# Optimization experiments

Measured on AMD Instinct MI355X. Metric: run time of the kernel, lower is better.

Reference implementation:

```python
import jax, jax.numpy as jnp
import numpy as np


def setup_inputs() -> dict:
    key = jax.random.key(0)
    ks = jax.random.split(key, 9)
    B, C, H, W = 4, 256, 128, 128
    d = C // 8
    x = jax.random.normal(ks[0], (B, C, H, W), jnp.float32)
    wq = jax.random.normal(ks[1], (d, C), jnp.float32) * 0.05
    bq = jax.random.normal(ks[2], (d,), jnp.float32) * 0.05
    wk = jax.random.normal(ks[3], (d, C), jnp.float32) * 0.05
    bk = jax.random.normal(ks[4], (d,), jnp.float32) * 0.05
    wv = jax.random.normal(ks[5], (d, C), jnp.float32) * 0.05
    bv = jax.random.normal(ks[6], (d,), jnp.float32) * 0.05
    wp = jax.random.normal(ks[7], (C, d, 3, 3), jnp.float32) * 0.05
    gamma = jax.random.normal(ks[8], (1,), jnp.float32)
    return dict(x=x, wq=wq, bq=bq, wk=wk, bk=bk, wv=wv, bv=bv, wp=wp, gamma=gamma)


def reference(x, wq, bq, wk, bk, wv, bv, wp, gamma):
    B, C, H, W = x.shape
    d = wq.shape[0]  # C // 8
    N = H * W
    # 1x1 convs expressed as channel matmuls
    q = jnp.einsum('bchw,dc->bdhw', x, wq) + bq[None, :, None, None]
    k = jnp.einsum('bchw,dc->bdhw', x, wk) + bk[None, :, None, None]
    v = jnp.einsum('bchw,dc->bdhw', x, wv) + bv[None, :, None, None]
    Q = q.reshape(B, d, N)
    K = k.reshape(B, d, N)
    V = v.reshape(B, d, N)
    # channel-channel energy: [B, d, d]
    energy = jnp.einsum('bdn,ben->bde', Q, K)
    energy_new = jnp.max(energy, axis=-1, keepdims=True) - energy
    attention = jax.nn.softmax(energy_new, axis=-1)
    out = jnp.einsum('bde,ben->bdn', attention, V).reshape(B, d, H, W)
    # 3x3 conv (no bias) + exact GELU
    out = jax.lax.conv_general_dilated(
        out, wp, window_strides=(1, 1), padding='SAME',
        dimension_numbers=('NCHW', 'OIHW', 'NCHW'))
    out = jax.nn.gelu(out, approximate=False)
    return gamma[0] * out + x
```

## Files before the change

kernel.cpp:

```cpp
#include <hip/hip_runtime.h>
#include <hip/hip_bf16.h>
#include <math.h>

#define BB 4
#define CC 256
#define HH 128
#define WW 128
#define NN (HH*WW)
#define DD 32

#define AOT_CI   44
#define AOT_ROWE (130*AOT_CI)
#define AOT_IMGE (130*AOT_ROWE)
#define AOT_BYTES ((size_t)BB*AOT_IMGE*2)
#define AOT_ALLOC (AOT_BYTES + 1024)

#define WT_BYTES (9*256*AOT_CI*2)

#define PATCH_SZ 45760
#define WSLAB    22528
#define CONV_LDS (PATCH_SZ + 2*WSLAB)
#define EPI_PITCH 260

#define ASWZ_BYTES 98304
#define QKPITCH 36

typedef __attribute__((ext_vector_type(8)))  short bf16x8;
typedef __attribute__((ext_vector_type(4)))  float f32x4;
typedef __attribute__((ext_vector_type(16))) float f32x16;

__device__ inline void async_copy16(void* lds, const void* g) {
    __builtin_amdgcn_global_load_lds(
        (const __attribute__((address_space(1))) unsigned int*)g,
        (__attribute__((address_space(3))) unsigned int*)lds, 16, 0, 0);
}

__device__ inline unsigned short f2bf(float f) {
    __hip_bfloat16 h = __float2bfloat16(f);
    return *reinterpret_cast<unsigned short*>(&h);
}

__device__ inline void split2(float v, unsigned short& h, unsigned short& l) {
    __hip_bfloat16 hb = __float2bfloat16(v);
    float r = v - __bfloat162float(hb);
    __hip_bfloat16 lb = __float2bfloat16(r);
    h = *reinterpret_cast<unsigned short*>(&hb);
    l = *reinterpret_cast<unsigned short*>(&lb);
}

__device__ inline bf16x8 ld_frag8(const char* p) {
    union { bf16x8 v; short4 h[2]; } u;
    u.h[0] = *(const short4*)(p);
    u.h[1] = *(const short4*)(p + 8);
    return u.v;
}

__device__ inline float gelu_fast(float v) {
    float a = fabsf(v) * 0.70710678118654752f;
    float t = __fdividef(1.0f, fmaf(0.3275911f, a, 1.0f));
    float p = t * fmaf(t, fmaf(t, fmaf(t, fmaf(t, 1.061405429f, -1.453152027f),
                                       1.421413741f), -0.284496736f), 0.254829592f);
    float e = 1.0f - p * __expf(-a * a);
    float erfv = (v < 0.0f) ? -e : e;
    return 0.5f * v * (1.0f + erfv);
}

__global__ __launch_bounds__(256) void prep_kernel(
    const float* __restrict__ wp, unsigned short* __restrict__ Wt,
    const float* __restrict__ wq, const float* __restrict__ wk,
    const float* __restrict__ wv, unsigned short* __restrict__ Aswz,
    unsigned short* __restrict__ AOT)
{
    const int blk = blockIdx.x;
    if (blk < 288) {
        int i = blk*256 + threadIdx.x;
        int kk = i / (256*32);
        int r  = i % (256*32);
        int co = r >> 5, ci = r & 31;
        float v = wp[((size_t)co*32 + ci)*9 + kk];
        Wt[((size_t)kk*256 + co)*AOT_CI + ci] = f2bf(v);
    } else if (blk < 480) {
        int i = (blk-288)*256 + threadIdx.x;
        int j    = i & 7;
        int lane = (i >> 3) & 63;
        int cf   = (i >> 9) % 3;
        int s    = i / 1536;
        int row  = cf*32 + (lane & 31);
        int k    = s*16 + (lane >> 5)*8 + j;
        int c    = k >> 1;
        float w  = (row < 32) ? wq[row*256 + c]
                 : (row < 64) ? wk[(row-32)*256 + c]
                              : wv[(row-64)*256 + c];
        unsigned short h, l;
        split2(w, h, l);
        Aswz[i] = (k & 1) ? l : h;
    } else {
        int idx = (blk-480)*256 + threadIdx.x;
        if (idx < BB*22704) {
            int b = idx / 22704;
            int r = idx % 22704;
            size_t off;
            if (r < 11440) {
                int row = (r < 5720) ? 0 : 129;
                int e   = (r < 5720) ? r : r - 5720;
                off = (size_t)b*AOT_IMGE + (size_t)row*AOT_ROWE + e;
            } else {
                int r2 = r - 11440;
                int rr = r2 / 88 + 1;
                int w2 = r2 % 88;
                int col = (w2 < 44) ? 0 : 129;
                int ci  = (w2 < 44) ? w2 : w2 - 44;
                off = (size_t)b*AOT_IMGE + (size_t)rr*AOT_ROWE
                    + (size_t)col*AOT_CI + ci;
            }
            AOT[off] = 0;
        }
    }
}

__global__ __launch_bounds__(256) void qkv_mfma_kernel(
    const float* __restrict__ x, const unsigned short* __restrict__ Aswz,
    const float* __restrict__ bq, const float* __restrict__ bk,
    const float* __restrict__ bv,
    float* __restrict__ Vout, float* __restrict__ Ep)
{
    __shared__ __align__(16) float lds_f[4*3072 + 96];
    const int b    = blockIdx.y;
    const int s    = blockIdx.x;
    const int n0   = s * 32;
    const int tid  = threadIdx.x;
    const int w    = tid >> 6;
    const int lane = tid & 63;
    const int l31  = lane & 31;
    const int lh   = lane >> 5;

    float* biasL = lds_f + 12288;
    if (tid < 96)
        biasL[tid] = (tid < 32) ? bq[tid] : (tid < 64) ? bk[tid-32] : bv[tid-64];

    const float* xlane = x + ((size_t)b*CC + 64*w + 4*lh)*NN + (n0 + l31);
    const bf16x8* Ab = (const bf16x8*)Aswz;
    const int st0 = 8*w;

    float xq[8][4];
    #pragma unroll
    for (int p = 0; p < 8; ++p) {
        const float* pp = xlane + (size_t)(8*p)*NN;
        xq[p][0] = pp[0];            xq[p][1] = pp[(size_t)NN];
        xq[p][2] = pp[(size_t)2*NN]; xq[p][3] = pp[(size_t)3*NN];
    }
    bf16x8 aq[2][3];
    #pragma unroll
    for (int p = 0; p < 2; ++p) {
        aq[p][0] = Ab[((st0+p)*3 + 0)*64 + lane];
        aq[p][1] = Ab[((st0+p)*3 + 1)*64 + lane];
        aq[p][2] = Ab[((st0+p)*3 + 2)*64 + lane];
    }

    f32x16 acc0 = {0}, acc1 = {0}, acc2 = {0};
    #pragma unroll
    for (int ph = 0; ph < 8; ++ph) {
        bf16x8 a0 = aq[ph & 1][0];
        bf16x8 a1 = aq[ph & 1][1];
        bf16x8 a2 = aq[ph & 1][2];
        if (ph < 6) {
            aq[ph & 1][0] = Ab[((st0+ph+2)*3 + 0)*64 + lane];
            aq[ph & 1][1] = Ab[((st0+ph+2)*3 + 1)*64 + lane];
            aq[ph & 1][2] = Ab[((st0+ph+2)*3 + 2)*64 + lane];
        }
        union { bf16x8 v; unsigned int u[4]; } B1, B2;
        #pragma unroll
        for (int j = 0; j < 4; ++j) {
            float vj = xq[ph][j];
            unsigned int hb = __float_as_uint(vj) & 0xFFFF0000u;
            float rj = vj - __uint_as_float(hb);
            unsigned int lb = __float_as_uint(rj) >> 16;
            B1.u[j] = hb | (hb >> 16);
            B2.u[j] = lb | (lb << 16);
        }
        acc0 = __builtin_amdgcn_mfma_f32_32x32x16_bf16(a0, B1.v, acc0, 0, 0, 0);
        acc1 = __builtin_amdgcn_mfma_f32_32x32x16_bf16(a1, B1.v, acc1, 0, 0, 0);
        acc2 = __builtin_amdgcn_mfma_f32_32x32x16_bf16(a2, B1.v, acc2, 0, 0, 0);
        acc0 = __builtin_amdgcn_mfma_f32_32x32x16_bf16(a0, B2.v, acc0, 0, 0, 0);
        acc1 = __builtin_amdgcn_mfma_f32_32x32x16_bf16(a1, B2.v, acc1, 0, 0, 0);
        acc2 = __builtin_amdgcn_mfma_f32_32x32x16_bf16(a2, B2.v, acc2, 0, 0, 0);
    }

    float* slab = lds_f + w*3072;
    #pragma unroll
    for (int r = 0; r < 16; ++r) {
        slab[(     r)*64 + lane] = acc0[r];
        slab[(16 + r)*64 + lane] = acc1[r];
        slab[(32 + r)*64 + lane] = acc2[r];
    }
    __syncthreads();

    float sums[12];
    #pragma unroll
    for (int i = 0; i < 12; ++i) {
        const int idx = tid + i*256;
        const int row = idx >> 5, n = idx & 31;
        const int cf = row >> 5, rsub = row & 31;
        const int r   = ((rsub >> 3) << 2) | (rsub & 3);
        const int lh2 = (rsub >> 2) & 1;
        const int fo  = (cf*16 + r)*64 + lh2*32 + n;
        sums[i] = lds_f[fo] + lds_f[3072 + fo] + lds_f[6144 + fo]
                + lds_f[9216 + fo] + biasL[row];
    }
    __syncthreads();

    #pragma unroll
    for (int i = 0; i < 12; ++i) {
        const int idx = tid + i*256;
        const int row = idx >> 5, n = idx & 31;
        if (row < 64)
            lds_f[row*QKPITCH + n] = sums[i];
        else
            Vout[((size_t)b*DD + (row-64))*NN + n0 + n] = sums[i];
    }
    __syncthreads();

    const int d  = tid >> 3;
    const int e0 = tid & 7;
    const float* qrow = lds_f + d*QKPITCH;
    float s0 = 0.f, s1 = 0.f, s2 = 0.f, s3 = 0.f;
    #pragma unroll
    for (int n4 = 0; n4 < 32; n4 += 4) {
        float4 qv = *(const float4*)(qrow + n4);
        float4 k0 = *(const float4*)(lds_f + (32 + e0     )*QKPITCH + n4);
        float4 k1 = *(const float4*)(lds_f + (32 + e0 +  8)*QKPITCH + n4);
        float4 k2 = *(const float4*)(lds_f + (32 + e0 + 16)*QKPITCH + n4);
        float4 k3 = *(const float4*)(lds_f + (32 + e0 + 24)*QKPITCH + n4);
        s0 += qv.x*k0.x + qv.y*k0.y + qv.z*k0.z + qv.w*k0.w;
        s1 += qv.x*k1.x + qv.y*k1.y + qv.z*k1.z + qv.w*k1.w;
        s2 += qv.x*k2.x + qv.y*k2.y + qv.z*k2.z + qv.w*k2.w;
        s3 += qv.x*k3.x + qv.y*k3.y + qv.z*k3.z + qv.w*k3.w;
    }
    float* ep = Ep + ((size_t)s*BB + b)*1024;
    ep[d*32 + e0]      = s0;
    ep[d*32 + e0 + 8]  = s1;
    ep[d*32 + e0 + 16] = s2;
    ep[d*32 + e0 + 24] = s3;
}

__global__ __launch_bounds__(256) void ereduce_kernel(
    const float* __restrict__ Ep, float* __restrict__ Epr)
{
    const int b = blockIdx.y, S = blockIdx.x;
    const int t = threadIdx.x;
    float4 a = {0.f, 0.f, 0.f, 0.f};
    #pragma unroll
    for (int p = 0; p < 8; ++p) {
        float4 v = *(const float4*)(Ep + ((size_t)(S*8 + p)*BB + b)*1024 + t*4);
        a.x += v.x; a.y += v.y; a.z += v.z; a.w += v.w;
    }
    *(float4*)(Epr + ((size_t)S*BB + b)*1024 + t*4) = a;
}

__global__ __launch_bounds__(1024) void softmax_kernel(
    const float* __restrict__ Ep, float* __restrict__ attT)
{
    const int b = blockIdx.x;
    const int e = threadIdx.x, d = threadIdx.y;
    float s = 0.f;
    for (int p = 0; p < 64; ++p)
        s += Ep[((size_t)p * BB + b) * (DD * DD) + d * DD + e];
    float nv = -s;
    float m = nv;
    for (int off = 16; off > 0; off >>= 1) m = fmaxf(m, __shfl_xor(m, off, 32));
    float pe = expf(nv - m);
    float su = pe;
    for (int off = 16; off > 0; off >>= 1) su += __shfl_xor(su, off, 32);
    attT[(size_t)b * (DD * DD) + e * DD + d] = pe / su;
}

__global__ __launch_bounds__(256) void pv_kernel(
    const float* __restrict__ V, const float* __restrict__ attT,
    unsigned short* __restrict__ AOT)
{
    __shared__ float Vs[DD][128];
    __shared__ float at4[DD][DD];
    const int b  = blockIdx.y;
    const int n0 = blockIdx.x * 128;
    const int tid = threadIdx.x;
    for (int i = tid; i < 1024; i += 256) {
        int r = i >> 5, c4 = i & 31;
        *(float4*)&Vs[r][c4*4] =
            *(const float4*)(V + ((size_t)b*DD + r)*NN + n0 + c4*4);
    }
    for (int i = tid; i < 1024; i += 256)
        at4[i >> 5][i & 31] = attT[(size_t)b*1024 + i];
    __syncthreads();
    const int nl = tid & 127;
    const int dg = tid >> 7;
    float acc[16];
    #pragma unroll
    for (int k = 0; k < 16; ++k) acc[k] = 0.f;
    #pragma unroll 4
    for (int e = 0; e < DD; ++e) {
        float v = Vs[e][nl];
        const float4* ar = (const float4*)&at4[e][dg*16];
        #pragma unroll
        for (int q = 0; q < 4; ++q) {
            float4 a = ar[q];
            acc[4*q+0] += a.x * v; acc[4*q+1] += a.y * v;
            acc[4*q+2] += a.z * v; acc[4*q+3] += a.w * v;
        }
    }
    const int n = n0 + nl;
    const int h = n >> 7, w = n & 127;
    unsigned short* dst = AOT + (size_t)b*AOT_IMGE + (size_t)(h+1)*AOT_ROWE
                              + (size_t)(w+1)*AOT_CI + dg*16;
    #pragma unroll
    for (int q = 0; q < 4; ++q) {
        ushort4 u;
        u.x = f2bf(acc[4*q+0]); u.y = f2bf(acc[4*q+1]);
        u.z = f2bf(acc[4*q+2]); u.w = f2bf(acc[4*q+3]);
        *(ushort4*)(dst + 4*q) = u;
    }
}

__global__ __launch_bounds__(512, 1) void conv_kernel(
    const unsigned short* __restrict__ AOT, const unsigned short* __restrict__ Wt,
    const float* __restrict__ gammap, const float* __restrict__ x,
    float* __restrict__ out)
{
    __shared__ __align__(16) char lds[CONV_LDS];
    const int b   = blockIdx.y;
    const int h0  = blockIdx.x * 2;
    const int tid = threadIdx.x;
    const int wid = tid >> 6;
    const int lane = tid & 63;
    const int l15 = lane & 15;
    const int lj  = lane >> 4;
    const int wn  = wid & 1;
    const int wc  = wid >> 1;

    const char* psrc = (const char*)(AOT + (size_t)b*AOT_IMGE + (size_t)h0*AOT_ROWE);
    for (int i = tid; i < PATCH_SZ/16; i += 512)
        async_copy16(lds + i*16, psrc + i*16);
    for (int i = tid; i < WSLAB/16; i += 512)
        async_copy16(lds + PATCH_SZ + i*16, (const char*)Wt + i*16);
    __syncthreads();

    f32x4 acc[4][8];
    #pragma unroll
    for (int cf = 0; cf < 4; ++cf)
        #pragma unroll
        for (int nf = 0; nf < 8; ++nf)
            acc[cf][nf] = (f32x4){0.f, 0.f, 0.f, 0.f};

    for (int kk = 0; kk < 9; ++kk) {
        if (kk < 8) {
            const char* wsrc = (const char*)Wt + (size_t)(kk+1)*WSLAB;
            char* wdst = lds + PATCH_SZ + ((kk+1)&1)*WSLAB;
            for (int i = tid; i < WSLAB/16; i += 512)
                async_copy16(wdst + i*16, wsrc + i*16);
        }
        const int kh = kk / 3, kw = kk % 3;
        const char* wbase = lds + PATCH_SZ + (kk&1)*WSLAB;
        bf16x8 af[4];
        #pragma unroll
        for (int cf = 0; cf < 4; ++cf)
            af[cf] = ld_frag8(wbase + (wc*64 + cf*16 + l15)*88 + lj*16);
        #pragma unroll
        for (int nf = 0; nf < 8; ++nf) {
            const int cell = (wn + kh)*130 + nf*16 + l15 + kw;
            const bf16x8 bfr = ld_frag8(lds + cell*88 + lj*16);
            #pragma unroll
            for (int cf = 0; cf < 4; ++cf)
                acc[cf][nf] = __builtin_amdgcn_mfma_f32_16x16x32_bf16(
                    af[cf], bfr, acc[cf][nf], 0, 0, 0);
        }
        __syncthreads();
    }

    const float g0 = gammap[0];
    float* lf = (float*)lds;
    for (int k = 0; k < 4; ++k) {
        if (wc == k) {
            #pragma unroll
            for (int cf = 0; cf < 4; ++cf) {
                const int rl = cf*16 + 4*lj;
                #pragma unroll
                for (int nf = 0; nf < 8; ++nf) {
                    const int col = wn*128 + nf*16 + l15;
                    #pragma unroll
                    for (int j = 0; j < 4; ++j)
                        lf[(rl + j)*EPI_PITCH + col] = acc[cf][nf][j];
                }
            }
        }
        __syncthreads();
        #pragma unroll
        for (int it = 0; it < 8; ++it) {
            const int idx = tid + it*512;
            const int row = idx >> 6, c4 = idx & 63;
            const int co  = k*64 + row;
            const size_t g = ((size_t)b*CC + co)*NN + (size_t)h0*WW + c4*4;
            float4 v  = *(const float4*)(lf + row*EPI_PITCH + c4*4);
            float4 xv = *(const float4*)(x + g);
            float4 o;
            o.x = g0*gelu_fast(v.x) + xv.x;
            o.y = g0*gelu_fast(v.y) + xv.y;
            o.z = g0*gelu_fast(v.z) + xv.z;
            o.w = g0*gelu_fast(v.w) + xv.w;
            *(float4*)(out + g) = o;
        }
        __syncthreads();
    }
}

extern "C" void kernel_launch(void* const* d_in, const int* in_sizes, int n_in,
                              void* d_out, int out_size, void* d_ws, size_t ws_size,
                              hipStream_t stream)
{
    const float* x  = (const float*)d_in[0];
    const float* wq = (const float*)d_in[1];
    const float* bq = (const float*)d_in[2];
    const float* wk = (const float*)d_in[3];
    const float* bk = (const float*)d_in[4];
    const float* wv = (const float*)d_in[5];
    const float* bv = (const float*)d_in[6];
    const float* wp = (const float*)d_in[7];
    const float* gm = (const float*)d_in[8];
    float* out = (float*)d_out;

    float* Vbuf = out;

    char* ws = (char*)d_ws;
    unsigned short* AOT  = (unsigned short*)ws;
    unsigned short* Wt   = (unsigned short*)(ws + AOT_ALLOC);
    unsigned short* Aswz = (unsigned short*)(ws + AOT_ALLOC + WT_BYTES);
    float* Ep  = (float*)(ws + AOT_ALLOC + WT_BYTES + ASWZ_BYTES);
    float* Epr = Ep + (size_t)512*BB*1024;
    float* ATT = Epr + (size_t)64*BB*1024;

    prep_kernel    <<<dim3(1024), 256, 0, stream>>>(wp, Wt, wq, wk, wv, Aswz, AOT);
    qkv_mfma_kernel<<<dim3(512, BB), 256, 0, stream>>>(x, Aswz, bq, bk, bv, Vbuf, Ep);
    ereduce_kernel <<<dim3(64, BB), 256, 0, stream>>>(Ep, Epr);
    softmax_kernel <<<dim3(BB), dim3(32, 32), 0, stream>>>(Epr, ATT);
    pv_kernel      <<<dim3(128, BB), 256, 0, stream>>>(Vbuf, ATT, AOT);
    conv_kernel    <<<dim3(64, BB), 512, 0, stream>>>(AOT, Wt, gm, x, out);
}
```

Baseline: 83.37 us.

## Widen QKV tile to 64 pixels with LDS-staged split-bf16 input and 2x2 wave split

The QKV projection kernel now handles 64 pixels per block instead of 32. Input x is loaded with coalesced float4 reads, pre-split into hi/lo bf16 pairs, and staged in LDS, and the four waves are arranged as 2 pixel halves by 2 channel halves. This halves the number of blocks and the partial-energy slabs the reduction kernel must process, and shrinks the cross-wave reduction from four slabs to two. In exchange it adds extra barriers and a two-round staging loop, and the launch bound now asks for three blocks per CU.

```diff
diff --git a/kernel.cpp b/kernel.cpp
--- a/kernel.cpp
+++ b/kernel.cpp
@@ -23,7 +23,7 @@
 #define EPI_PITCH 260
 
 #define ASWZ_BYTES 98304
-#define QKPITCH 36
+#define QKP5 68
 
 typedef __attribute__((ext_vector_type(8)))  short bf16x8;
 typedef __attribute__((ext_vector_type(4)))  float f32x4;
@@ -46,6 +46,14 @@
     __hip_bfloat16 lb = __float2bfloat16(r);
     h = *reinterpret_cast<unsigned short*>(&hb);
     l = *reinterpret_cast<unsigned short*>(&lb);
+}
+
+__device__ inline unsigned int packsplit(float v) {
+    unsigned int fb = __float_as_uint(v);
+    unsigned int hb = fb & 0xFFFF0000u;
+    float r = v - __uint_as_float(hb);
+    unsigned int lb = __float_as_uint(r) >> 16;
+    return (hb >> 16) | (lb << 16);
 }
 
 __device__ inline bf16x8 ld_frag8(const char* p) {
@@ -118,119 +126,138 @@
     }
 }
 
-__global__ __launch_bounds__(256) void qkv_mfma_kernel(
+__global__ __launch_bounds__(256, 3) void qkv_mfma_kernel(
     const float* __restrict__ x, const unsigned short* __restrict__ Aswz,
     const float* __restrict__ bq, const float* __restrict__ bk,
     const float* __restrict__ bv,
     float* __restrict__ Vout, float* __restrict__ Ep)
 {
-    __shared__ __align__(16) float lds_f[4*3072 + 96];
+    __shared__ __align__(16) float lds_f[8192 + 96];
     const int b    = blockIdx.y;
     const int s    = blockIdx.x;
-    const int n0   = s * 32;
+    const int n0   = s * 64;
     const int tid  = threadIdx.x;
     const int w    = tid >> 6;
     const int lane = tid & 63;
     const int l31  = lane & 31;
     const int lh   = lane >> 5;
-
-    float* biasL = lds_f + 12288;
+    const int wn   = w & 1;
+    const int wk   = w >> 1;
+
+    float* biasL = lds_f + 8192;
     if (tid < 96)
         biasL[tid] = (tid < 32) ? bq[tid] : (tid < 64) ? bk[tid-32] : bv[tid-64];
 
-    const float* xlane = x + ((size_t)b*CC + 64*w + 4*lh)*NN + (n0 + l31);
+    unsigned int* stage = (unsigned int*)lds_f;
     const bf16x8* Ab = (const bf16x8*)Aswz;
-    const int st0 = 8*w;
-
-    float xq[8][4];
-    #pragma unroll
-    for (int p = 0; p < 8; ++p) {
-        const float* pp = xlane + (size_t)(8*p)*NN;
-        xq[p][0] = pp[0];            xq[p][1] = pp[(size_t)NN];
-        xq[p][2] = pp[(size_t)2*NN]; xq[p][3] = pp[(size_t)3*NN];
-    }
-    bf16x8 aq[2][3];
-    #pragma unroll
-    for (int p = 0; p < 2; ++p) {
-        aq[p][0] = Ab[((st0+p)*3 + 0)*64 + lane];
-        aq[p][1] = Ab[((st0+p)*3 + 1)*64 + lane];
-        aq[p][2] = Ab[((st0+p)*3 + 2)*64 + lane];
-    }
 
     f32x16 acc0 = {0}, acc1 = {0}, acc2 = {0};
-    #pragma unroll
-    for (int ph = 0; ph < 8; ++ph) {
-        bf16x8 a0 = aq[ph & 1][0];
-        bf16x8 a1 = aq[ph & 1][1];
-        bf16x8 a2 = aq[ph & 1][2];
-        if (ph < 6) {
-            aq[ph & 1][0] = Ab[((st0+ph+2)*3 + 0)*64 + lane];
-            aq[ph & 1][1] = Ab[((st0+ph+2)*3 + 1)*64 + lane];
-            aq[ph & 1][2] = Ab[((st0+ph+2)*3 + 2)*64 + lane];
-        }
-        union { bf16x8 v; unsigned int u[4]; } B1, B2;
-        #pragma unroll
-        for (int j = 0; j < 4; ++j) {
-            float vj = xq[ph][j];
-            unsigned int hb = __float_as_uint(vj) & 0xFFFF0000u;
-            float rj = vj - __uint_as_float(hb);
-            unsigned int lb = __float_as_uint(rj) >> 16;
-            B1.u[j] = hb | (hb >> 16);
-            B2.u[j] = lb | (lb << 16);
-        }
-        acc0 = __builtin_amdgcn_mfma_f32_32x32x16_bf16(a0, B1.v, acc0, 0, 0, 0);
-        acc1 = __builtin_amdgcn_mfma_f32_32x32x16_bf16(a1, B1.v, acc1, 0, 0, 0);
-        acc2 = __builtin_amdgcn_mfma_f32_32x32x16_bf16(a2, B1.v, acc2, 0, 0, 0);
-        acc0 = __builtin_amdgcn_mfma_f32_32x32x16_bf16(a0, B2.v, acc0, 0, 0, 0);
-        acc1 = __builtin_amdgcn_mfma_f32_32x32x16_bf16(a1, B2.v, acc1, 0, 0, 0);
-        acc2 = __builtin_amdgcn_mfma_f32_32x32x16_bf16(a2, B2.v, acc2, 0, 0, 0);
-    }
-
-    float* slab = lds_f + w*3072;
-    #pragma unroll
-    for (int r = 0; r < 16; ++r) {
-        slab[(     r)*64 + lane] = acc0[r];
-        slab[(16 + r)*64 + lane] = acc1[r];
-        slab[(32 + r)*64 + lane] = acc2[r];
-    }
-    __syncthreads();
-
-    float sums[12];
-    #pragma unroll
-    for (int i = 0; i < 12; ++i) {
-        const int idx = tid + i*256;
-        const int row = idx >> 5, n = idx & 31;
-        const int cf = row >> 5, rsub = row & 31;
-        const int r   = ((rsub >> 3) << 2) | (rsub & 3);
-        const int lh2 = (rsub >> 2) & 1;
-        const int fo  = (cf*16 + r)*64 + lh2*32 + n;
-        sums[i] = lds_f[fo] + lds_f[3072 + fo] + lds_f[6144 + fo]
-                + lds_f[9216 + fo] + biasL[row];
-    }
-    __syncthreads();
-
-    #pragma unroll
-    for (int i = 0; i < 12; ++i) {
-        const int idx = tid + i*256;
-        const int row = idx >> 5, n = idx & 31;
-        if (row < 64)
-            lds_f[row*QKPITCH + n] = sums[i];
-        else
-            Vout[((size_t)b*DD + (row-64))*NN + n0 + n] = sums[i];
+
+    for (int r = 0; r < 2; ++r) {
+        if (r) __syncthreads();
+        #pragma unroll
+        for (int i = 0; i < 8; ++i) {
+            const int idx  = i*256 + tid;
+            const int cidx = idx >> 10;
+            const int rem  = idx & 1023;
+            const int chl  = rem >> 4;
+            const int f4   = rem & 15;
+            const float4 v4 = *(const float4*)(
+                x + ((size_t)b*CC + cidx*128 + r*64 + chl)*NN + n0 + f4*4);
+            uint4 u;
+            u.x = packsplit(v4.x); u.y = packsplit(v4.y);
+            u.z = packsplit(v4.z); u.w = packsplit(v4.w);
+            *(uint4*)(stage + cidx*4096 + chl*64 + f4*4) = u;
+        }
+        __syncthreads();
+        bf16x8 aq[2][3];
+        {
+            const int sg0 = wk*16 + r*8;
+            #pragma unroll
+            for (int p = 0; p < 2; ++p) {
+                aq[p][0] = Ab[((sg0+p)*3 + 0)*64 + lane];
+                aq[p][1] = Ab[((sg0+p)*3 + 1)*64 + lane];
+                aq[p][2] = Ab[((sg0+p)*3 + 2)*64 + lane];
+            }
+        }
+        #pragma unroll
+        for (int st = 0; st < 8; ++st) {
+            const int st_g = wk*16 + r*8 + st;
+            bf16x8 a0 = aq[st & 1][0];
+            bf16x8 a1 = aq[st & 1][1];
+            bf16x8 a2 = aq[st & 1][2];
+            if (st < 6) {
+                aq[st & 1][0] = Ab[((st_g+2)*3 + 0)*64 + lane];
+                aq[st & 1][1] = Ab[((st_g+2)*3 + 1)*64 + lane];
+                aq[st & 1][2] = Ab[((st_g+2)*3 + 2)*64 + lane];
+            }
+            unsigned int u0 = stage[wk*4096 + (8*st + 4*lh + 0)*64 + 32*wn + l31];
+            unsigned int u1 = stage[wk*4096 + (8*st + 4*lh + 1)*64 + 32*wn + l31];
+            unsigned int u2 = stage[wk*4096 + (8*st + 4*lh + 2)*64 + 32*wn + l31];
+            unsigned int u3 = stage[wk*4096 + (8*st + 4*lh + 3)*64 + 32*wn + l31];
+            union { bf16x8 v; unsigned int d[4]; } B1, B2;
+            B1.d[0] = (u0 << 16) | (u0 & 0xFFFFu);
+            B1.d[1] = (u1 << 16) | (u1 & 0xFFFFu);
+            B1.d[2] = (u2 << 16) | (u2 & 0xFFFFu);
+            B1.d[3] = (u3 << 16) | (u3 & 0xFFFFu);
+            B2.d[0] = (u0 & 0xFFFF0000u) | (u0 >> 16);
+            B2.d[1] = (u1 & 0xFFFF0000u) | (u1 >> 16);
+            B2.d[2] = (u2 & 0xFFFF0000u) | (u2 >> 16);
+            B2.d[3] = (u3 & 0xFFFF0000u) | (u3 >> 16);
+            acc0 = __builtin_amdgcn_mfma_f32_32x32x16_bf16(a0, B1.v, acc0, 0, 0, 0);
+            acc1 = __builtin_amdgcn_mfma_f32_32x32x16_bf16(a1, B1.v, acc1, 0, 0, 0);
+            acc2 = __builtin_amdgcn_mfma_f32_32x32x16_bf16(a2, B1.v, acc2, 0, 0, 0);
+            acc0 = __builtin_amdgcn_mfma_f32_32x32x16_bf16(a0, B2.v, acc0, 0, 0, 0);
+            acc1 = __builtin_amdgcn_mfma_f32_32x32x16_bf16(a1, B2.v, acc1, 0, 0, 0);
+            acc2 = __builtin_amdgcn_mfma_f32_32x32x16_bf16(a2, B2.v, acc2, 0, 0, 0);
+        }
+    }
+
+    __syncthreads();
+    if (wk == 1) {
+        float* slab = lds_f + wn*3072;
+        #pragma unroll
+        for (int r = 0; r < 16; ++r) {
+            slab[(     r)*64 + lane] = acc0[r];
+            slab[(16 + r)*64 + lane] = acc1[r];
+            slab[(32 + r)*64 + lane] = acc2[r];
+        }
+    }
+    __syncthreads();
+    float sq[16], sk[16], sv[16];
+    if (wk == 0) {
+        const float* slab = lds_f + wn*3072;
+        #pragma unroll
+        for (int r = 0; r < 16; ++r) {
+            const int rsub = (r & 3) + 8*(r >> 2) + 4*lh;
+            sq[r] = acc0[r] + slab[(     r)*64 + lane] + biasL[rsub];
+            sk[r] = acc1[r] + slab[(16 + r)*64 + lane] + biasL[32 + rsub];
+            sv[r] = acc2[r] + slab[(32 + r)*64 + lane] + biasL[64 + rsub];
+        }
+    }
+    __syncthreads();
+    if (wk == 0) {
+        #pragma unroll
+        for (int r = 0; r < 16; ++r) {
+            const int rsub = (r & 3) + 8*(r >> 2) + 4*lh;
+            lds_f[rsub*QKP5      + 32*wn + l31] = sq[r];
+            lds_f[(32+rsub)*QKP5 + 32*wn + l31] = sk[r];
+            Vout[((size_t)b*DD + rsub)*NN + n0 + 32*wn + l31] = sv[r];
+        }
     }
     __syncthreads();
 
     const int d  = tid >> 3;
     const int e0 = tid & 7;
-    const float* qrow = lds_f + d*QKPITCH;
+    const float* qrow = lds_f + d*QKP5;
     float s0 = 0.f, s1 = 0.f, s2 = 0.f, s3 = 0.f;
     #pragma unroll
-    for (int n4 = 0; n4 < 32; n4 += 4) {
+    for (int n4 = 0; n4 < 64; n4 += 4) {
         float4 qv = *(const float4*)(qrow + n4);
-        float4 k0 = *(const float4*)(lds_f + (32 + e0     )*QKPITCH + n4);
-        float4 k1 = *(const float4*)(lds_f + (32 + e0 +  8)*QKPITCH + n4);
-        float4 k2 = *(const float4*)(lds_f + (32 + e0 + 16)*QKPITCH + n4);
-        float4 k3 = *(const float4*)(lds_f + (32 + e0 + 24)*QKPITCH + n4);
+        float4 k0 = *(const float4*)(lds_f + (32 + e0     )*QKP5 + n4);
+        float4 k1 = *(const float4*)(lds_f + (32 + e0 +  8)*QKP5 + n4);
+        float4 k2 = *(const float4*)(lds_f + (32 + e0 + 16)*QKP5 + n4);
+        float4 k3 = *(const float4*)(lds_f + (32 + e0 + 24)*QKP5 + n4);
         s0 += qv.x*k0.x + qv.y*k0.y + qv.z*k0.z + qv.w*k0.w;
         s1 += qv.x*k1.x + qv.y*k1.y + qv.z*k1.z + qv.w*k1.w;
         s2 += qv.x*k2.x + qv.y*k2.y + qv.z*k2.z + qv.w*k2.w;
@@ -263,7 +290,8 @@
     const int b = blockIdx.x;
     const int e = threadIdx.x, d = threadIdx.y;
     float s = 0.f;
-    for (int p = 0; p < 64; ++p)
+    #pragma unroll
+    for (int p = 0; p < 32; ++p)
         s += Ep[((size_t)p * BB + b) * (DD * DD) + d * DD + e];
     float nv = -s;
     float m = nv;
@@ -308,9 +336,9 @@
         }
     }
     const int n = n0 + nl;
-    const int h = n >> 7, w = n & 127;
+    const int h = n >> 7, ww = n & 127;
     unsigned short* dst = AOT + (size_t)b*AOT_IMGE + (size_t)(h+1)*AOT_ROWE
-                              + (size_t)(w+1)*AOT_CI + dg*16;
+                              + (size_t)(ww+1)*AOT_CI + dg*16;
     #pragma unroll
     for (int q = 0; q < 4; ++q) {
         ushort4 u;
@@ -433,12 +461,12 @@
     unsigned short* Wt   = (unsigned short*)(ws + AOT_ALLOC);
     unsigned short* Aswz = (unsigned short*)(ws + AOT_ALLOC + WT_BYTES);
     float* Ep  = (float*)(ws + AOT_ALLOC + WT_BYTES + ASWZ_BYTES);
-    float* Epr = Ep + (size_t)512*BB*1024;
-    float* ATT = Epr + (size_t)64*BB*1024;
+    float* Epr = Ep + (size_t)256*BB*1024;
+    float* ATT = Epr + (size_t)32*BB*1024;
 
     prep_kernel    <<<dim3(1024), 256, 0, stream>>>(wp, Wt, wq, wk, wv, Aswz, AOT);
-    qkv_mfma_kernel<<<dim3(512, BB), 256, 0, stream>>>(x, Aswz, bq, bk, bv, Vbuf, Ep);
-    ereduce_kernel <<<dim3(64, BB), 256, 0, stream>>>(Ep, Epr);
+    qkv_mfma_kernel<<<dim3(256, BB), 256, 0, stream>>>(x, Aswz, bq, bk, bv, Vbuf, Ep);
+    ereduce_kernel <<<dim3(32, BB), 256, 0, stream>>>(Ep, Epr);
     softmax_kernel <<<dim3(BB), dim3(32, 32), 0, stream>>>(Epr, ATT);
     pv_kernel      <<<dim3(128, BB), 256, 0, stream>>>(Vbuf, ATT, AOT);
     conv_kernel    <<<dim3(64, BB), 512, 0, stream>>>(AOT, Wt, gm, x, out);
```

Result: faster. 81.07 us (-2.8%).
